# Optimization experiments

Hardware: AMD Instinct MI355X
Metric: run time of the kernel (lower is better)

Reference implementation:

```python
import jax, jax.numpy as jnp
import numpy as np

N_NODES = 100000
N_EDGES = 1600000
IN_DIM = 4
HID = 64


def gcn_conv(x, src, dst, W, b, num_nodes):
    """PyG GCNConv: out = D^-1/2 (A+I) D^-1/2 (x @ W) + b, add aggregation."""
    loop = jnp.arange(num_nodes)
    src_f = jnp.concatenate([src, loop])  # [E+N]
    dst_f = jnp.concatenate([dst, loop])
    # degree from destination (col) counts, self loops included -> deg >= 1
    deg = jax.ops.segment_sum(jnp.ones_like(dst_f, dtype=x.dtype), dst_f,
                              num_segments=num_nodes)
    dinv = jax.lax.rsqrt(deg)
    norm = dinv[src_f] * dinv[dst_f]  # [E+N]
    h = x @ W  # [N, out] transform first (cheaper when out <= in is false too; matches PyG)
    msg = h[src_f] * norm[:, None]  # [E+N, out]
    out = jax.ops.segment_sum(msg, dst_f, num_segments=num_nodes)
    return out + b


def setup_inputs() -> dict:
    key = jax.random.key(0)
    ks = jax.random.split(key, 6)
    x = jax.random.normal(ks[0], (N_NODES, IN_DIM), dtype=jnp.float32)
    edge_index = jax.random.randint(ks[1], (2, N_EDGES), 0, N_NODES, dtype=jnp.int64)
    # glorot-ish scaled weights
    W1 = jax.random.normal(ks[2], (IN_DIM, HID), dtype=jnp.float32) / np.sqrt(IN_DIM)
    b1 = jnp.zeros((HID,), dtype=jnp.float32)
    W2 = jax.random.normal(ks[3], (HID, HID), dtype=jnp.float32) / np.sqrt(HID)
    b2 = jnp.zeros((HID,), dtype=jnp.float32)
    Wl = jax.random.normal(ks[4], (HID, 1), dtype=jnp.float32) / np.sqrt(HID)
    bl = jnp.zeros((1,), dtype=jnp.float32)
    return {"x": x, "edge_index": edge_index, "W1": W1, "b1": b1,
            "W2": W2, "b2": b2, "Wl": Wl, "bl": bl}


def reference(x, edge_index, W1, b1, W2, b2, Wl, bl):
    num_nodes = x.shape[0]
    src, dst = edge_index[0], edge_index[1]
    h = jax.nn.relu(gcn_conv(x, src, dst, W1, b1, num_nodes))
    h = jax.nn.relu(gcn_conv(h, src, dst, W2, b2, num_nodes))
    logits = (h @ Wl + bl).squeeze(-1)  # [N]
    return logits
```

## Files before the change

### kernel.cpp

```cpp
#include <hip/hip_runtime.h>

#define NN 100000
#define NE 1600000
#define HID 64
#define NBUK 391
#define SRCBITS 17
#define SRCMASK 0x1FFFF
#define EBLK 4096
#define GE2 ((NE + EBLK - 1) / EBLK)
#define BSTRIDE 6144
#define CSTRIDE 8192

typedef __attribute__((ext_vector_type(8))) short bf16x8;
typedef __attribute__((ext_vector_type(4))) float f32x4;

__device__ __forceinline__ unsigned short f2bf(float f) {
    unsigned int x = __float_as_uint(f);
    return (unsigned short)((x + 0x7FFFu + ((x >> 16) & 1u)) >> 16);
}
__device__ __forceinline__ float bflo(unsigned int u) { return __uint_as_float(u << 16); }
__device__ __forceinline__ float bfhi(unsigned int u) { return __uint_as_float(u & 0xFFFF0000u); }

__global__ void k_prep(const float* __restrict__ W2, unsigned short* __restrict__ w2t,
                       float* __restrict__ xs, unsigned short* __restrict__ hs) {
    int t = threadIdx.x;
    for (int i = t; i < 4096; i += 256) {
        int k = i >> 6, n = i & 63;
        w2t[n * 72 + k] = f2bf(W2[i]);
    }
    if (t < 64) hs[NN * 64 + t] = 0;
    if (t == 64) ((float4*)xs)[NN] = make_float4(0.f, 0.f, 0.f, 0.f);
}

__global__ void __launch_bounds__(256)
k_fill1(const int* __restrict__ ei, int* __restrict__ gcnt,
        unsigned int* __restrict__ bbuf) {
    __shared__ int s_src[EBLK];
    __shared__ int s_dst[EBLK];
    __shared__ int s_hist[NBUK];
    __shared__ int s_flag;
    int t = threadIdx.x;
    int b = blockIdx.x;

    for (int i = t; i < NBUK; i += 256) s_hist[i] = 0;
    if (t < 64) {
        unsigned long long bal = __ballot(ei[2 * t + 1] != 0);
        if (t == 0) s_flag = (bal == 0ULL) ? 1 : 0;
    }
    __syncthreads();
    int f = s_flag;
    int base = b * EBLK;
    int m = NE - base; if (m > EBLK) m = EBLK;

    if (f) {
        const int4* ps = (const int4*)ei;
        const int4* pd = (const int4*)(ei + 2 * (size_t)NE);
#pragma unroll
        for (int k = 0; k < EBLK / 512; ++k) {
            int e = base + k * 512 + t * 2;
            if (e < NE) {
                int4 vs = ps[e >> 1];
                int4 vd = pd[e >> 1];
                int l = e - base;
                s_src[l] = vs.x;     s_dst[l] = vd.x;
                s_src[l + 1] = vs.z; s_dst[l + 1] = vd.z;
                atomicAdd(&s_hist[vd.x >> 8], 1);
                atomicAdd(&s_hist[vd.z >> 8], 1);
            }
        }
    } else {
        const int4* ps = (const int4*)ei;
        const int4* pd = (const int4*)(ei + NE);
#pragma unroll
        for (int k = 0; k < EBLK / 1024; ++k) {
            int e = base + k * 1024 + t * 4;
            if (e < NE) {
                int4 vs = ps[e >> 2];
                int4 vd = pd[e >> 2];
                int l = e - base;
                s_src[l] = vs.x; s_src[l + 1] = vs.y; s_src[l + 2] = vs.z; s_src[l + 3] = vs.w;
                s_dst[l] = vd.x; s_dst[l + 1] = vd.y; s_dst[l + 2] = vd.z; s_dst[l + 3] = vd.w;
                atomicAdd(&s_hist[vd.x >> 8], 1);
                atomicAdd(&s_hist[vd.y >> 8], 1);
                atomicAdd(&s_hist[vd.z >> 8], 1);
                atomicAdd(&s_hist[vd.w >> 8], 1);
            }
        }
    }
    __syncthreads();
    for (int i = t; i < NBUK; i += 256) {
        int c = s_hist[i];
        int r = c ? atomicAdd(&gcnt[i], c) : 0;
        s_hist[i] = i * BSTRIDE + r;
    }
    __syncthreads();
    for (int e = t; e < m; e += 256) {
        int d = s_dst[e];
        int p = atomicAdd(&s_hist[d >> 8], 1);
        bbuf[p] = ((unsigned int)(d & 255) << SRCBITS) | (unsigned int)s_src[e];
    }
}

__global__ void __launch_bounds__(256)
k_passB(const unsigned int* __restrict__ bbuf, const int* __restrict__ gcnt,
        const float* __restrict__ x, int* __restrict__ meta,
        float* __restrict__ dinv, float* __restrict__ xs, int* __restrict__ csr) {
    __shared__ int hist[256];
    __shared__ int scn[256];
    __shared__ int cur[256];
    int t = threadIdx.x;
    int b = blockIdx.x;
    int sz = gcnt[b];
    const unsigned int* buf = bbuf + (size_t)b * BSTRIDE;
    hist[t] = 0;
    __syncthreads();
    for (int e = t; e < sz; e += 256)
        atomicAdd(&hist[buf[e] >> SRCBITS], 1);
    __syncthreads();
    int deg = hist[t];
    int pdeg = (deg + 7) & ~7;
    scn[t] = pdeg; __syncthreads();
    for (int off = 1; off < 256; off <<= 1) {
        int u = (t >= off) ? scn[t - off] : 0;
        __syncthreads();
        scn[t] += u;
        __syncthreads();
    }
    int myoff = b * CSTRIDE + scn[t] - pdeg;
    int node = b * 256 + t;
    if (node < NN) {
        int dcl = deg < 255 ? deg : 255;
        meta[node] = ((myoff >> 2) << 8) | dcl;
        float d = 1.0f / sqrtf((float)(deg + 1));
        dinv[node] = d;
        float4 xv = ((const float4*)x)[node];
        float4 o; o.x = d * xv.x; o.y = d * xv.y; o.z = d * xv.z; o.w = d * xv.w;
        ((float4*)xs)[node] = o;
    }
    for (int p = deg; p < pdeg; ++p) csr[myoff + p] = NN;
    cur[t] = myoff;
    __syncthreads();
    for (int e = t; e < sz; e += 256) {
        unsigned int u = buf[e];
        int p = atomicAdd(&cur[u >> SRCBITS], 1);
        csr[p] = (int)(u & SRCMASK);
    }
}

__global__ void k_mm2(const float* __restrict__ xs, const int* __restrict__ meta,
                      const int* __restrict__ csr, const float* __restrict__ dinv,
                      const float* __restrict__ W1, const float* __restrict__ b1,
                      const unsigned short* __restrict__ w2t, unsigned short* __restrict__ hs) {
    __shared__ unsigned short h1b[64 * 72];
    __shared__ float4 sPart[256];
    __shared__ float4 sAgg[64];
    __shared__ float4 sXs[64];
    __shared__ float sW1[256];
    __shared__ float sb1[64];
    __shared__ float sdv[64];
    __shared__ int smeta[64];
    int t = threadIdx.x;
    int base = blockIdx.x * 64;
    if (t < 64) {
        int g = base + t;
        bool ok = (g < NN);
        smeta[t] = ok ? meta[g] : 0;
        sdv[t]  = ok ? dinv[g] : 0.f;
        sXs[t]  = ok ? ((const float4*)xs)[g] : make_float4(0.f, 0.f, 0.f, 0.f);
        sb1[t]  = b1[t];
    }
    sW1[t] = W1[t];
    __syncthreads();
    {
        int node_l = t & 63, part = t >> 6;
        int mv = smeta[node_l];
        int n = mv & 255;
        int nb = mv >> 8;
        const int4* cp4 = (const int4*)csr;
        float4 s = make_float4(0.f, 0.f, 0.f, 0.f);
        for (int c = part; c * 4 < n; c += 4) {
            int4 q = cp4[nb + c];
            float4 v0 = ((const float4*)xs)[q.x];
            float4 v1 = ((const float4*)xs)[q.y];
            float4 v2 = ((const float4*)xs)[q.z];
            float4 v3 = ((const float4*)xs)[q.w];
            s.x += (v0.x + v1.x) + (v2.x + v3.x);
            s.y += (v0.y + v1.y) + (v2.y + v3.y);
            s.z += (v0.z + v1.z) + (v2.z + v3.z);
            s.w += (v0.w + v1.w) + (v2.w + v3.w);
        }
        sPart[t] = s;
    }
    __syncthreads();
    if (t < 64) {
        float4 a = sPart[t], b = sPart[t + 64], c = sPart[t + 128], d = sPart[t + 192];
        float4 xi = sXs[t];
        float dn = sdv[t];
        float4 o;
        o.x = dn * (a.x + b.x + c.x + d.x + xi.x);
        o.y = dn * (a.y + b.y + c.y + d.y + xi.y);
        o.z = dn * (a.z + b.z + c.z + d.z + xi.z);
        o.w = dn * (a.w + b.w + c.w + d.w + xi.w);
        sAgg[t] = o;
    }
    __syncthreads();
#pragma unroll
    for (int i = 0; i < 16; ++i) {
        int e = i * 256 + t;
        int nl = e >> 6, c = e & 63;
        float4 a = sAgg[nl];
        float h = fmaf(a.x, sW1[c], fmaf(a.y, sW1[64 + c],
                  fmaf(a.z, sW1[128 + c], fmaf(a.w, sW1[192 + c], sb1[c]))));
        h1b[nl * 72 + c] = f2bf(fmaxf(h, 0.f));
    }
    __syncthreads();
    int w = t >> 6, lane = t & 63, l15 = lane & 15, quad = lane >> 4;
    bf16x8 a0 = *(const bf16x8*)&h1b[(w * 16 + l15) * 72 + quad * 8];
    bf16x8 a1 = *(const bf16x8*)&h1b[(w * 16 + l15) * 72 + 32 + quad * 8];
    f32x4 acc[4];
#pragma unroll
    for (int nt = 0; nt < 4; ++nt) {
        bf16x8 bb0 = *(const bf16x8*)&w2t[(nt * 16 + l15) * 72 + quad * 8];
        bf16x8 bb1 = *(const bf16x8*)&w2t[(nt * 16 + l15) * 72 + 32 + quad * 8];
        f32x4 c = {0.f, 0.f, 0.f, 0.f};
        c = __builtin_amdgcn_mfma_f32_16x16x32_bf16(a0, bb0, c, 0, 0, 0);
        c = __builtin_amdgcn_mfma_f32_16x16x32_bf16(a1, bb1, c, 0, 0, 0);
        acc[nt] = c;
    }
#pragma unroll
    for (int nt = 0; nt < 4; ++nt) {
#pragma unroll
        for (int r = 0; r < 4; ++r) {
            int localn = w * 16 + quad * 4 + r;
            int g = base + localn;
            if (g < NN) hs[g * 64 + nt * 16 + l15] = f2bf(acc[nt][r] * sdv[localn]);
        }
    }
}

__global__ void k_gather_head(const unsigned short* __restrict__ hs, const int* __restrict__ meta,
                              const int* __restrict__ csr, const float* __restrict__ dinv,
                              const float* __restrict__ b2, const float* __restrict__ Wl,
                              const float* __restrict__ bl, float* __restrict__ out) {
    int t = threadIdx.x;
    int c = t & 63;
    int g = c >> 4;
    int sl = c & 15;
    int node = blockIdx.x * 16 + (t >> 6) * 4 + g;
    int mv = meta[node];
    int n = mv & 255;
    int nb = mv >> 8;
    const uint2* hrow = (const uint2*)hs;
    const int4* cp4 = (const int4*)csr;
    float4 A = make_float4(0.f, 0.f, 0.f, 0.f);
#define ACC2(u) do { \
    A.x += bflo(u.x); A.y += bfhi(u.x); A.z += bflo(u.y); A.w += bfhi(u.y); } while (0)
    for (int j8 = 0; j8 * 8 < n; ++j8) {
        int4 q0 = cp4[nb + 2 * j8];
        int4 q1 = cp4[nb + 2 * j8 + 1];
        uint2 u0 = hrow[q0.x * 16 + sl];
        uint2 u1 = hrow[q0.y * 16 + sl];
        uint2 u2 = hrow[q0.z * 16 + sl];
        uint2 u3 = hrow[q0.w * 16 + sl];
        uint2 u4 = hrow[q1.x * 16 + sl];
        uint2 u5 = hrow[q1.y * 16 + sl];
        uint2 u6 = hrow[q1.z * 16 + sl];
        uint2 u7 = hrow[q1.w * 16 + sl];
        ACC2(u0); ACC2(u1); ACC2(u2); ACC2(u3);
        ACC2(u4); ACC2(u5); ACC2(u6); ACC2(u7);
    }
    uint2 uS = hrow[node * 16 + sl];
    ACC2(uS);
#undef ACC2
    float4 bv = ((const float4*)b2)[sl];
    float4 wv = ((const float4*)Wl)[sl];
    float dn = dinv[node];
    float v = fmaxf(fmaf(dn, A.x, bv.x), 0.f) * wv.x
            + fmaxf(fmaf(dn, A.y, bv.y), 0.f) * wv.y
            + fmaxf(fmaf(dn, A.z, bv.z), 0.f) * wv.z
            + fmaxf(fmaf(dn, A.w, bv.w), 0.f) * wv.w;
    v += __shfl_xor(v, 1, 64);
    v += __shfl_xor(v, 2, 64);
    v += __shfl_xor(v, 4, 64);
    v += __shfl_xor(v, 8, 64);
    if (sl == 0) out[node] = v + bl[0];
}

extern "C" void kernel_launch(void* const* d_in, const int* in_sizes, int n_in,
                              void* d_out, int out_size, void* d_ws, size_t ws_size,
                              hipStream_t stream) {
    const float* x  = (const float*)d_in[0];
    const int*   ei = (const int*)d_in[1];
    const float* W1 = (const float*)d_in[2];
    const float* b1 = (const float*)d_in[3];
    const float* W2 = (const float*)d_in[4];
    const float* b2 = (const float*)d_in[5];
    const float* Wl = (const float*)d_in[6];
    const float* bl = (const float*)d_in[7];
    float* out = (float*)d_out;

    char* w = (char*)d_ws;
    float* dinv  = (float*)w;                  w += NN * 4;
    int*   metaA = (int*)w;                    w += NN * 4;
    float* xs    = (float*)w;                  w += (size_t)(NN + 1) * 16;
    unsigned short* hs = (unsigned short*)w;   w += (size_t)(NN + 1) * HID * 2;
    unsigned short* w2t = (unsigned short*)w;  w += ((64 * 72 * 2 + 255) & ~255);
    int*   gcnt  = (int*)w;                    w += ((NBUK + 63) & ~63) * 4;
    int*   csr   = (int*)w;                    w += (size_t)NBUK * CSTRIDE * 4;
    w = (char*)(((size_t)w + 255) & ~(size_t)255);
    unsigned int* bbuf = (unsigned int*)w;     w += (size_t)NBUK * BSTRIDE * 4;

    hipMemsetAsync(gcnt, 0, NBUK * sizeof(int), stream);
    hipLaunchKernelGGL(k_prep,  dim3(1),    dim3(256), 0, stream, W2, w2t, xs, hs);
    hipLaunchKernelGGL(k_fill1, dim3(GE2),  dim3(256), 0, stream, ei, gcnt, bbuf);
    hipLaunchKernelGGL(k_passB, dim3(NBUK), dim3(256), 0, stream,
                       bbuf, gcnt, x, metaA, dinv, xs, csr);
    hipLaunchKernelGGL(k_mm2, dim3((NN + 63) / 64), dim3(256), 0, stream,
                       xs, metaA, csr, dinv, W1, b1, w2t, hs);
    hipLaunchKernelGGL(k_gather_head, dim3(NN / 16), dim3(256), 0, stream,
                       hs, metaA, csr, dinv, b2, Wl, bl, out);
}
```

Before: 184.4 us.

## Drop prep kernel, convert W2 per block, unroll gather by sixteen

Removes the single-block k_prep launch. Sentinel-row zeroing moves into block 0 of k_fill1, and every k_mm2 block now converts W2 to transposed bf16 in shared memory itself. CSR rows are padded to multiples of 16 so the layer-2 gather loop can issue 16 independent neighbor loads per iteration instead of 8. The trade-offs are redundant W2 conversion in each of about 1563 blocks, extra LDS per block, more padded sentinel reads for low-degree nodes, and CSR slots that may overflow CSTRIDE.

```diff
diff --git a/kernel.cpp b/kernel.cpp
--- a/kernel.cpp
+++ b/kernel.cpp
@@ -21,20 +21,10 @@
 __device__ __forceinline__ float bflo(unsigned int u) { return __uint_as_float(u << 16); }
 __device__ __forceinline__ float bfhi(unsigned int u) { return __uint_as_float(u & 0xFFFF0000u); }
 
-__global__ void k_prep(const float* __restrict__ W2, unsigned short* __restrict__ w2t,
-                       float* __restrict__ xs, unsigned short* __restrict__ hs) {
-    int t = threadIdx.x;
-    for (int i = t; i < 4096; i += 256) {
-        int k = i >> 6, n = i & 63;
-        w2t[n * 72 + k] = f2bf(W2[i]);
-    }
-    if (t < 64) hs[NN * 64 + t] = 0;
-    if (t == 64) ((float4*)xs)[NN] = make_float4(0.f, 0.f, 0.f, 0.f);
-}
-
 __global__ void __launch_bounds__(256)
 k_fill1(const int* __restrict__ ei, int* __restrict__ gcnt,
-        unsigned int* __restrict__ bbuf) {
+        unsigned int* __restrict__ bbuf, float* __restrict__ xs,
+        unsigned short* __restrict__ hs) {
     __shared__ int s_src[EBLK];
     __shared__ int s_dst[EBLK];
     __shared__ int s_hist[NBUK];
@@ -42,6 +32,10 @@
     int t = threadIdx.x;
     int b = blockIdx.x;
 
+    if (b == 0) {
+        if (t < 64) hs[NN * 64 + t] = 0;
+        if (t == 64) ((float4*)xs)[NN] = make_float4(0.f, 0.f, 0.f, 0.f);
+    }
     for (int i = t; i < NBUK; i += 256) s_hist[i] = 0;
     if (t < 64) {
         unsigned long long bal = __ballot(ei[2 * t + 1] != 0);
@@ -118,7 +112,7 @@
         atomicAdd(&hist[buf[e] >> SRCBITS], 1);
     __syncthreads();
     int deg = hist[t];
-    int pdeg = (deg + 7) & ~7;
+    int pdeg = (deg + 15) & ~15;
     scn[t] = pdeg; __syncthreads();
     for (int off = 1; off < 256; off <<= 1) {
         int u = (t >= off) ? scn[t - off] : 0;
@@ -150,8 +144,9 @@
 __global__ void k_mm2(const float* __restrict__ xs, const int* __restrict__ meta,
                       const int* __restrict__ csr, const float* __restrict__ dinv,
                       const float* __restrict__ W1, const float* __restrict__ b1,
-                      const unsigned short* __restrict__ w2t, unsigned short* __restrict__ hs) {
+                      const float* __restrict__ W2, unsigned short* __restrict__ hs) {
     __shared__ unsigned short h1b[64 * 72];
+    __shared__ unsigned short w2t[64 * 72];
     __shared__ float4 sPart[256];
     __shared__ float4 sAgg[64];
     __shared__ float4 sXs[64];
@@ -170,6 +165,10 @@
         sb1[t]  = b1[t];
     }
     sW1[t] = W1[t];
+    for (int i = t; i < 4096; i += 256) {
+        int k = i >> 6, n = i & 63;
+        w2t[n * 72 + k] = f2bf(W2[i]);
+    }
     __syncthreads();
     {
         int node_l = t & 63, part = t >> 6;
@@ -255,19 +254,31 @@
     float4 A = make_float4(0.f, 0.f, 0.f, 0.f);
 #define ACC2(u) do { \
     A.x += bflo(u.x); A.y += bfhi(u.x); A.z += bflo(u.y); A.w += bfhi(u.y); } while (0)
-    for (int j8 = 0; j8 * 8 < n; ++j8) {
-        int4 q0 = cp4[nb + 2 * j8];
-        int4 q1 = cp4[nb + 2 * j8 + 1];
-        uint2 u0 = hrow[q0.x * 16 + sl];
-        uint2 u1 = hrow[q0.y * 16 + sl];
-        uint2 u2 = hrow[q0.z * 16 + sl];
-        uint2 u3 = hrow[q0.w * 16 + sl];
-        uint2 u4 = hrow[q1.x * 16 + sl];
-        uint2 u5 = hrow[q1.y * 16 + sl];
-        uint2 u6 = hrow[q1.z * 16 + sl];
-        uint2 u7 = hrow[q1.w * 16 + sl];
-        ACC2(u0); ACC2(u1); ACC2(u2); ACC2(u3);
-        ACC2(u4); ACC2(u5); ACC2(u6); ACC2(u7);
+    for (int j16 = 0; j16 * 16 < n; ++j16) {
+        int4 q0 = cp4[nb + 4 * j16];
+        int4 q1 = cp4[nb + 4 * j16 + 1];
+        int4 q2 = cp4[nb + 4 * j16 + 2];
+        int4 q3 = cp4[nb + 4 * j16 + 3];
+        uint2 u0  = hrow[q0.x * 16 + sl];
+        uint2 u1  = hrow[q0.y * 16 + sl];
+        uint2 u2  = hrow[q0.z * 16 + sl];
+        uint2 u3  = hrow[q0.w * 16 + sl];
+        uint2 u4  = hrow[q1.x * 16 + sl];
+        uint2 u5  = hrow[q1.y * 16 + sl];
+        uint2 u6  = hrow[q1.z * 16 + sl];
+        uint2 u7  = hrow[q1.w * 16 + sl];
+        uint2 u8  = hrow[q2.x * 16 + sl];
+        uint2 u9  = hrow[q2.y * 16 + sl];
+        uint2 u10 = hrow[q2.z * 16 + sl];
+        uint2 u11 = hrow[q2.w * 16 + sl];
+        uint2 u12 = hrow[q3.x * 16 + sl];
+        uint2 u13 = hrow[q3.y * 16 + sl];
+        uint2 u14 = hrow[q3.z * 16 + sl];
+        uint2 u15 = hrow[q3.w * 16 + sl];
+        ACC2(u0);  ACC2(u1);  ACC2(u2);  ACC2(u3);
+        ACC2(u4);  ACC2(u5);  ACC2(u6);  ACC2(u7);
+        ACC2(u8);  ACC2(u9);  ACC2(u10); ACC2(u11);
+        ACC2(u12); ACC2(u13); ACC2(u14); ACC2(u15);
     }
     uint2 uS = hrow[node * 16 + sl];
     ACC2(uS);
@@ -304,19 +315,17 @@
     int*   metaA = (int*)w;                    w += NN * 4;
     float* xs    = (float*)w;                  w += (size_t)(NN + 1) * 16;
     unsigned short* hs = (unsigned short*)w;   w += (size_t)(NN + 1) * HID * 2;
-    unsigned short* w2t = (unsigned short*)w;  w += ((64 * 72 * 2 + 255) & ~255);
     int*   gcnt  = (int*)w;                    w += ((NBUK + 63) & ~63) * 4;
     int*   csr   = (int*)w;                    w += (size_t)NBUK * CSTRIDE * 4;
     w = (char*)(((size_t)w + 255) & ~(size_t)255);
     unsigned int* bbuf = (unsigned int*)w;     w += (size_t)NBUK * BSTRIDE * 4;
 
     hipMemsetAsync(gcnt, 0, NBUK * sizeof(int), stream);
-    hipLaunchKernelGGL(k_prep,  dim3(1),    dim3(256), 0, stream, W2, w2t, xs, hs);
-    hipLaunchKernelGGL(k_fill1, dim3(GE2),  dim3(256), 0, stream, ei, gcnt, bbuf);
+    hipLaunchKernelGGL(k_fill1, dim3(GE2),  dim3(256), 0, stream, ei, gcnt, bbuf, xs, hs);
     hipLaunchKernelGGL(k_passB, dim3(NBUK), dim3(256), 0, stream,
                        bbuf, gcnt, x, metaA, dinv, xs, csr);
     hipLaunchKernelGGL(k_mm2, dim3((NN + 63) / 64), dim3(256), 0, stream,
-                       xs, metaA, csr, dinv, W1, b1, w2t, hs);
+                       xs, metaA, csr, dinv, W1, b1, W2, hs);
     hipLaunchKernelGGL(k_gather_head, dim3(NN / 16), dim3(256), 0, stream,
                        hs, metaA, csr, dinv, b2, Wl, bl, out);
 }
```

After: 181.6 us. No clear change (-1.5%).
